# Performance work log

Hardware: AMD Instinct MI355X
Metric: run time of the kernel (lower is better)

Reference implementation:

```python
import jax, jax.numpy as jnp
import numpy as np

B, T, F, H, S = 4096, 200, 76, 128, 17


def setup_inputs() -> dict:
    key = jax.random.key(0)
    ks = jax.random.split(key, 10)
    kf = 1.0 / np.sqrt(H)
    return {
        "x": jax.random.normal(ks[0], (B, T, F), dtype=jnp.float32),
        "static": jax.random.normal(ks[1], (B, S), dtype=jnp.float32),
        "h0": jax.random.normal(ks[2], (B, H), dtype=jnp.float32),
        "c0": jax.random.normal(ks[3], (B, H), dtype=jnp.float32),
        "W_ih": jax.random.uniform(ks[4], (4 * H, F), jnp.float32, -kf, kf),
        "W_hh": jax.random.uniform(ks[5], (4 * H, H), jnp.float32, -kf, kf),
        "b_ih": jax.random.uniform(ks[6], (4 * H,), jnp.float32, -kf, kf),
        "b_hh": jax.random.uniform(ks[7], (4 * H,), jnp.float32, -kf, kf),
        "W_lin": jax.random.uniform(ks[8], (1, H + S), jnp.float32, -kf, kf),
        "b_lin": jax.random.uniform(ks[9], (1,), jnp.float32, -kf, kf),
    }


def reference(x, static, h0, c0, W_ih, W_hh, b_ih, b_hh, W_lin, b_lin):
    # Precompute input projections for all timesteps in one big GEMM: [B,T,4H]
    x_proj = jnp.einsum("btf,gf->btg", x, W_ih) + b_ih
    xs = jnp.swapaxes(x_proj, 0, 1)  # time-major [T, B, 4H]

    def step(carry, xp):
        h, c = carry
        gates = xp + h @ W_hh.T + b_hh  # [B, 4H]
        i, f, g, o = jnp.split(gates, 4, axis=-1)
        i, f, o = jax.nn.sigmoid(i), jax.nn.sigmoid(f), jax.nn.sigmoid(o)
        c = f * c + i * jnp.tanh(g)
        h = o * jnp.tanh(c)
        return (h, c), None

    (h, c), _ = jax.lax.scan(step, (h0, c0), xs)
    full = jnp.concatenate([h, static], axis=1)  # [B, H+S]
    predictions = full @ W_lin.T + b_lin  # [B, 1]
    return predictions
```

## Files before the change

kernel.cpp:

```cpp
#include <hip/hip_runtime.h>
#include <hip/hip_bf16.h>

#define B_TOT   4096
#define T_LEN   200
#define F_IN    76
#define H_DIM   128
#define S_DIM   17
#define BLK_B   16
#define NTHREADS 512
#define NT_CHUNK 8
#define NCHUNK  (T_LEN / NT_CHUNK)
#define XPITCH  96
#define HPITCH  136
#define ROW_F4  ((NT_CHUNK * F_IN) / 4)
#define PF_N    5

static_assert(NCHUNK * NT_CHUNK == T_LEN, "chunking must cover T exactly");

using f32x4 = __attribute__((ext_vector_type(4))) float;
using s16x8 = __attribute__((ext_vector_type(8))) short;

#if __has_builtin(__builtin_amdgcn_exp2f)
#define EXP2(v) __builtin_amdgcn_exp2f(v)
#else
#define EXP2(v) exp2f(v)
#endif
#if __has_builtin(__builtin_amdgcn_rcpf)
#define RCP(v) __builtin_amdgcn_rcpf(v)
#else
#define RCP(v) (1.0f / (v))
#endif

__device__ __forceinline__ short f2bf(float f) {
    union { float f; unsigned u; } v; v.f = f;
    unsigned r = v.u + 0x7FFFu + ((v.u >> 16) & 1u);
    return (short)(r >> 16);
}
__device__ __forceinline__ float bf2f(short s) {
    union { unsigned u; float f; } v;
    v.u = ((unsigned)(unsigned short)s) << 16;
    return v.f;
}
__device__ __forceinline__ unsigned cvt_pk_bf16(float lo, float hi) {
    unsigned r;
    asm("v_cvt_pk_bf16_f32 %0, %1, %2" : "=v"(r) : "v"(lo), "v"(hi));
    return r;
}

__global__ __launch_bounds__(NTHREADS, 2) void lstm_fused(
    const float* __restrict__ x,    const float* __restrict__ stat,
    const float* __restrict__ h0,   const float* __restrict__ c0,
    const float* __restrict__ W_ih, const float* __restrict__ W_hh,
    const float* __restrict__ b_ih, const float* __restrict__ b_hh,
    const float* __restrict__ W_lin, const float* __restrict__ b_lin,
    float* __restrict__ out)
{
    __shared__ __align__(16) short xbuf[2][NT_CHUNK][BLK_B][XPITCH];
    __shared__ __align__(16) short hbuf[2][BLK_B][HPITCH];

    const int tid  = threadIdx.x;
    const int lane = tid & 63;
    const int wave = tid >> 6;
    const int lrow = lane & 15;
    const int lk8  = (lane >> 4) << 3;
    const int r0   = (lane >> 4) << 2;
    const int b0   = blockIdx.x * BLK_B;
    const int hb   = wave << 4;

    const float C1 = 1.44269504088896f;
    const float gs[4] = { -C1, -C1, -2.0f * C1, -C1 };

    s16x8 wih[4][3], whh[4][4];
    float bias[4];
#pragma unroll
    for (int nt = 0; nt < 4; ++nt) {
        const int col = nt * H_DIM + hb + lrow;
        const float s = gs[nt];
#pragma unroll
        for (int kt = 0; kt < 3; ++kt) {
            s16x8 f;
#pragma unroll
            for (int j = 0; j < 8; ++j) {
                int k = kt * 32 + lk8 + j;
                float v = (k < F_IN) ? W_ih[col * F_IN + k] * s : 0.0f;
                f[j] = f2bf(v);
            }
            wih[nt][kt] = f;
        }
#pragma unroll
        for (int kt = 0; kt < 4; ++kt) {
            s16x8 f;
#pragma unroll
            for (int j = 0; j < 8; ++j) {
                int k = kt * 32 + lk8 + j;
                f[j] = f2bf(W_hh[col * H_DIM + k] * s);
            }
            whh[nt][kt] = f;
        }
        bias[nt] = (b_ih[col] + b_hh[col]) * s;
    }

    float c[4];
#pragma unroll
    for (int r = 0; r < 4; ++r)
        c[r] = c0[(b0 + r0 + r) * H_DIM + hb + lrow];

    for (int i = tid; i < BLK_B * H_DIM; i += NTHREADS) {
        int row = i >> 7, cc = i & 127;
        hbuf[0][row][cc] = f2bf(h0[(b0 + row) * H_DIM + cc]);
    }
    for (int i = tid; i < 2 * NT_CHUNK * BLK_B * (XPITCH - F_IN); i += NTHREADS) {
        int rem = i;
        int f   = rem % (XPITCH - F_IN); rem /= (XPITCH - F_IN);
        int row = rem % BLK_B;           rem /= BLK_B;
        int tt  = rem % NT_CHUNK;        rem /= NT_CHUNK;
        xbuf[rem][tt][row][F_IN + f] = 0;
    }

    const int prow = tid >> 5;
    const int pidx = tid & 31;
    const float* psrc = x + (size_t)(b0 + prow) * (T_LEN * F_IN) + pidx * 4;
    int ldsoff[PF_N];
#pragma unroll
    for (int i = 0; i < PF_N; ++i) {
        int s4 = pidx + 32 * i;
        int q  = 4 * s4;
        int tp = (q * 863) >> 16;
        int f0 = q - 76 * tp;
        ldsoff[i] = (tp * BLK_B + prow) * XPITCH + f0;
    }

    f32x4 pf[PF_N];
    auto issue = [&](int ch) {
        const float* p = psrc + (size_t)ch * (NT_CHUNK * F_IN);
#pragma unroll
        for (int i = 0; i < PF_N; ++i)
            if (i < PF_N - 1 || pidx < ROW_F4 - 4 * 32)
                pf[i] = *(const f32x4*)(p + i * 128);
    };
    auto commit = [&](int buf) {
        short* xb0 = &xbuf[buf][0][0][0];
#pragma unroll
        for (int i = 0; i < PF_N; ++i)
            if (i < PF_N - 1 || pidx < ROW_F4 - 4 * 32) {
                unsigned lo = cvt_pk_bf16(pf[i].x, pf[i].y);
                unsigned hi = cvt_pk_bf16(pf[i].z, pf[i].w);
                unsigned long long v = ((unsigned long long)hi << 32) | lo;
                *(unsigned long long*)(xb0 + ldsoff[i]) = v;
            }
    };

    issue(0);
    commit(0);
    __syncthreads();

    s16x8 axr[3];
    f32x4 xa[4];
    auto load_ax = [&](int buf, int tt) {
#pragma unroll
        for (int kt = 0; kt < 3; ++kt)
            axr[kt] = *(const s16x8*)&xbuf[buf][tt][lrow][kt * 32 + lk8];
    };
    auto calc_xa = [&]() {
#pragma unroll
        for (int nt = 0; nt < 4; ++nt) {
            f32x4 t = (f32x4){ bias[nt], bias[nt], bias[nt], bias[nt] };
#pragma unroll
            for (int kt = 0; kt < 3; ++kt)
                t = __builtin_amdgcn_mfma_f32_16x16x32_bf16(axr[kt], wih[nt][kt], t, 0, 0, 0);
            xa[nt] = t;
        }
    };

    load_ax(0, 0);
    calc_xa();

#define STEP(CUR, TT)                                                          \
    {                                                                          \
        s16x8 ah[4];                                                           \
        _Pragma("unroll")                                                      \
        for (int kt = 0; kt < 4; ++kt)                                         \
            ah[kt] = *(const s16x8*)&hbuf[CUR][lrow][kt * 32 + lk8];           \
        f32x4 acc[4];                                                          \
        _Pragma("unroll")                                                      \
        for (int nt = 0; nt < 4; ++nt) {                                       \
            f32x4 t = xa[nt];                                                  \
            _Pragma("unroll")                                                  \
            for (int kt = 0; kt < 4; ++kt)                                     \
                t = __builtin_amdgcn_mfma_f32_16x16x32_bf16(ah[kt], whh[nt][kt], t, 0, 0, 0); \
            acc[nt] = t;                                                       \
        }                                                                      \
        if ((TT) < NT_CHUNK - 1) { load_ax(xc, (TT) + 1); calc_xa(); }         \
        float hv[4];                                                           \
        _Pragma("unroll")                                                      \
        for (int r = 0; r < 4; ++r) {                                          \
            float A  = EXP2(acc[0][r]);                                        \
            float Bv = EXP2(acc[1][r]);                                        \
            float E  = EXP2(acc[2][r]);                                        \
            float Dv = EXP2(acc[3][r]);                                        \
            float sE = 1.f - E, p3 = 1.f + E;                                  \
            float p1 = 1.f + A, p2 = 1.f + Bv;                                 \
            float q13 = p1 * p3;                                               \
            float num = fmaf(c[r], q13, sE * p2);                              \
            float cn  = num * RCP(q13 * p2);                                   \
            c[r] = cn;                                                         \
            float ea = fminf(cn * (-2.f * C1), 80.f);                          \
            float Ec = EXP2(ea);                                               \
            float sEc = 1.f - Ec, uEc = 1.f + Ec;                              \
            hv[r] = sEc * RCP((1.f + Dv) * uEc);                               \
        }                                                                      \
        if ((TT) == 0 && ch + 1 < NCHUNK) issue(ch + 1);                       \
        if ((TT) == NT_CHUNK - 1 && ch + 1 < NCHUNK) commit(xc ^ 1);           \
        unsigned q01 = cvt_pk_bf16(hv[0], hv[1]);                              \
        unsigned q23 = cvt_pk_bf16(hv[2], hv[3]);                              \
        unsigned short* hp = (unsigned short*)&hbuf[(CUR) ^ 1][r0][hb + lrow]; \
        hp[0 * HPITCH] = (unsigned short)q01;                                  \
        hp[1 * HPITCH] = (unsigned short)(q01 >> 16);                          \
        hp[2 * HPITCH] = (unsigned short)q23;                                  \
        hp[3 * HPITCH] = (unsigned short)(q23 >> 16);                          \
        __syncthreads();                                                       \
        if ((TT) == NT_CHUNK - 1 && ch + 1 < NCHUNK) {                         \
            load_ax(xc ^ 1, 0); calc_xa();                                     \
        }                                                                      \
    }

    for (int ch = 0; ch < NCHUNK; ++ch) {
        const int xc = ch & 1;
        for (int tt = 0; tt < NT_CHUNK; tt += 2) {
            STEP(0, tt)
            STEP(1, tt + 1)
        }
    }
#undef STEP

    if (tid < BLK_B) {
        const int row = tid;
        float a = b_lin[0];
        for (int k = 0; k < H_DIM; ++k)
            a += bf2f(hbuf[0][row][k]) * W_lin[k];
        for (int s = 0; s < S_DIM; ++s)
            a += stat[(b0 + row) * S_DIM + s] * W_lin[H_DIM + s];
        out[b0 + row] = a;
    }
}

extern "C" void kernel_launch(void* const* d_in, const int* in_sizes, int n_in,
                              void* d_out, int out_size, void* d_ws, size_t ws_size,
                              hipStream_t stream) {
    const float* xx   = (const float*)d_in[0];
    const float* st   = (const float*)d_in[1];
    const float* h0   = (const float*)d_in[2];
    const float* c0   = (const float*)d_in[3];
    const float* Wih  = (const float*)d_in[4];
    const float* Whh  = (const float*)d_in[5];
    const float* bih  = (const float*)d_in[6];
    const float* bhh  = (const float*)d_in[7];
    const float* Wlin = (const float*)d_in[8];
    const float* blin = (const float*)d_in[9];
    float* o = (float*)d_out;

    lstm_fused<<<B_TOT / BLK_B, NTHREADS, 0, stream>>>(
        xx, st, h0, c0, Wih, Whh, bih, bhh, Wlin, blin, o);
}
```

Measured before the change: 207.9 us.

## Interleave input-projection MFMAs with gate nonlinearities and use raw LDS barrier

Splits the next-step input projection (REBUILD) per gate tile and interleaves it with the per-row nonlinearity computations. The aim is to overlap MFMA latency with transcendental VALU work. The x-tile LDS load is issued earlier, before the recurrent MFMAs, and the h stores are split so half can be written early. The time loop over each chunk is fully unrolled, and __syncthreads is replaced by a raw s_waitcnt lgkmcnt(0) + s_barrier, which risks missing waits on global memory operations.

```diff
diff --git a/kernel.cpp b/kernel.cpp
--- a/kernel.cpp
+++ b/kernel.cpp
@@ -47,6 +47,8 @@
     return r;
 }
 
+#define LDS_BARRIER() asm volatile("s_waitcnt lgkmcnt(0)\n\ts_barrier" ::: "memory")
+
 __global__ __launch_bounds__(NTHREADS, 2) void lstm_fused(
     const float* __restrict__ x,    const float* __restrict__ stat,
     const float* __restrict__ h0,   const float* __restrict__ c0,
@@ -71,7 +73,7 @@
     const float gs[4] = { -C1, -C1, -2.0f * C1, -C1 };
 
     s16x8 wih[4][3], whh[4][4];
-    float bias[4];
+    f32x4 biasf[4];
 #pragma unroll
     for (int nt = 0; nt < 4; ++nt) {
         const int col = nt * H_DIM + hb + lrow;
@@ -97,7 +99,8 @@
             }
             whh[nt][kt] = f;
         }
-        bias[nt] = (b_ih[col] + b_hh[col]) * s;
+        float bv = (b_ih[col] + b_hh[col]) * s;
+        biasf[nt] = (f32x4){ bv, bv, bv, bv };
     }
 
     float c[4];
@@ -161,77 +164,85 @@
         for (int kt = 0; kt < 3; ++kt)
             axr[kt] = *(const s16x8*)&xbuf[buf][tt][lrow][kt * 32 + lk8];
     };
-    auto calc_xa = [&]() {
-#pragma unroll
-        for (int nt = 0; nt < 4; ++nt) {
-            f32x4 t = (f32x4){ bias[nt], bias[nt], bias[nt], bias[nt] };
-#pragma unroll
-            for (int kt = 0; kt < 3; ++kt)
-                t = __builtin_amdgcn_mfma_f32_16x16x32_bf16(axr[kt], wih[nt][kt], t, 0, 0, 0);
-            xa[nt] = t;
-        }
-    };
+
+#define REBUILD(NT)                                                              \
+    xa[NT] = __builtin_amdgcn_mfma_f32_16x16x32_bf16(axr[2], wih[NT][2],         \
+             __builtin_amdgcn_mfma_f32_16x16x32_bf16(axr[1], wih[NT][1],         \
+             __builtin_amdgcn_mfma_f32_16x16x32_bf16(axr[0], wih[NT][0],         \
+             biasf[NT], 0, 0, 0), 0, 0, 0), 0, 0, 0)
+
+#define NONLIN(R)                                                                \
+    {   float A  = EXP2(acc[0][R]);                                              \
+        float Bv = EXP2(acc[1][R]);                                              \
+        float E  = EXP2(acc[2][R]);                                              \
+        float Dv = EXP2(acc[3][R]);                                              \
+        float p1 = 1.f + A, p2 = 1.f + Bv, p3 = 1.f + E;                         \
+        float q13 = p1 * p3;                                                     \
+        float num = fmaf(c[R], q13, (1.f - E) * p2);                             \
+        float cn  = num * RCP(q13 * p2);                                         \
+        c[R] = cn;                                                               \
+        float Ec  = EXP2(fminf(cn * (-2.f * C1), 80.f));                         \
+        hv[R] = (1.f - Ec) * RCP((1.f + Dv) * (1.f + Ec)); }
 
     load_ax(0, 0);
-    calc_xa();
-
-#define STEP(CUR, TT)                                                          \
-    {                                                                          \
-        s16x8 ah[4];                                                           \
-        _Pragma("unroll")                                                      \
-        for (int kt = 0; kt < 4; ++kt)                                         \
-            ah[kt] = *(const s16x8*)&hbuf[CUR][lrow][kt * 32 + lk8];           \
-        f32x4 acc[4];                                                          \
-        _Pragma("unroll")                                                      \
-        for (int nt = 0; nt < 4; ++nt) {                                       \
-            f32x4 t = xa[nt];                                                  \
-            _Pragma("unroll")                                                  \
-            for (int kt = 0; kt < 4; ++kt)                                     \
-                t = __builtin_amdgcn_mfma_f32_16x16x32_bf16(ah[kt], whh[nt][kt], t, 0, 0, 0); \
-            acc[nt] = t;                                                       \
-        }                                                                      \
-        if ((TT) < NT_CHUNK - 1) { load_ax(xc, (TT) + 1); calc_xa(); }         \
-        float hv[4];                                                           \
-        _Pragma("unroll")                                                      \
-        for (int r = 0; r < 4; ++r) {                                          \
-            float A  = EXP2(acc[0][r]);                                        \
-            float Bv = EXP2(acc[1][r]);                                        \
-            float E  = EXP2(acc[2][r]);                                        \
-            float Dv = EXP2(acc[3][r]);                                        \
-            float sE = 1.f - E, p3 = 1.f + E;                                  \
-            float p1 = 1.f + A, p2 = 1.f + Bv;                                 \
-            float q13 = p1 * p3;                                               \
-            float num = fmaf(c[r], q13, sE * p2);                              \
-            float cn  = num * RCP(q13 * p2);                                   \
-            c[r] = cn;                                                         \
-            float ea = fminf(cn * (-2.f * C1), 80.f);                          \
-            float Ec = EXP2(ea);                                               \
-            float sEc = 1.f - Ec, uEc = 1.f + Ec;                              \
-            hv[r] = sEc * RCP((1.f + Dv) * uEc);                               \
-        }                                                                      \
-        if ((TT) == 0 && ch + 1 < NCHUNK) issue(ch + 1);                       \
-        if ((TT) == NT_CHUNK - 1 && ch + 1 < NCHUNK) commit(xc ^ 1);           \
-        unsigned q01 = cvt_pk_bf16(hv[0], hv[1]);                              \
-        unsigned q23 = cvt_pk_bf16(hv[2], hv[3]);                              \
-        unsigned short* hp = (unsigned short*)&hbuf[(CUR) ^ 1][r0][hb + lrow]; \
-        hp[0 * HPITCH] = (unsigned short)q01;                                  \
-        hp[1 * HPITCH] = (unsigned short)(q01 >> 16);                          \
-        hp[2 * HPITCH] = (unsigned short)q23;                                  \
-        hp[3 * HPITCH] = (unsigned short)(q23 >> 16);                          \
-        __syncthreads();                                                       \
-        if ((TT) == NT_CHUNK - 1 && ch + 1 < NCHUNK) {                         \
-            load_ax(xc ^ 1, 0); calc_xa();                                     \
-        }                                                                      \
-    }
-
+    REBUILD(0); REBUILD(1); REBUILD(2); REBUILD(3);
+
+#define STEP(CUR, TT)                                                            \
+    {                                                                            \
+        s16x8 ah[4];                                                             \
+        _Pragma("unroll")                                                        \
+        for (int kt = 0; kt < 4; ++kt)                                           \
+            ah[kt] = *(const s16x8*)&hbuf[CUR][lrow][kt * 32 + lk8];             \
+        if ((TT) < NT_CHUNK - 1) load_ax(xc, (TT) + 1);                          \
+        f32x4 acc[4];                                                            \
+        _Pragma("unroll")                                                        \
+        for (int nt = 0; nt < 4; ++nt) {                                         \
+            f32x4 t = __builtin_amdgcn_mfma_f32_16x16x32_bf16(ah[0], whh[nt][0], xa[nt], 0, 0, 0); \
+            t = __builtin_amdgcn_mfma_f32_16x16x32_bf16(ah[1], whh[nt][1], t, 0, 0, 0); \
+            t = __builtin_amdgcn_mfma_f32_16x16x32_bf16(ah[2], whh[nt][2], t, 0, 0, 0); \
+            t = __builtin_amdgcn_mfma_f32_16x16x32_bf16(ah[3], whh[nt][3], t, 0, 0, 0); \
+            acc[nt] = t;                                                         \
+        }                                                                        \
+        if ((TT) == 0 && ch + 1 < NCHUNK) issue(ch + 1);                         \
+        float hv[4];                                                             \
+        unsigned short* hp = (unsigned short*)&hbuf[(CUR) ^ 1][r0][hb + lrow];   \
+        NONLIN(0);                                                               \
+        if ((TT) < NT_CHUNK - 1) { REBUILD(0); }                                 \
+        NONLIN(1);                                                               \
+        {   unsigned q01 = cvt_pk_bf16(hv[0], hv[1]);                            \
+            hp[0 * HPITCH] = (unsigned short)q01;                                \
+            hp[1 * HPITCH] = (unsigned short)(q01 >> 16); }                      \
+        if ((TT) < NT_CHUNK - 1) { REBUILD(1); }                                 \
+        NONLIN(2);                                                               \
+        if ((TT) < NT_CHUNK - 1) { REBUILD(2); }                                 \
+        NONLIN(3);                                                               \
+        {   unsigned q23 = cvt_pk_bf16(hv[2], hv[3]);                            \
+            hp[2 * HPITCH] = (unsigned short)q23;                                \
+            hp[3 * HPITCH] = (unsigned short)(q23 >> 16); }                      \
+        if ((TT) < NT_CHUNK - 1) { REBUILD(3); }                                 \
+        if ((TT) == NT_CHUNK - 1 && ch + 1 < NCHUNK) commit(xc ^ 1);             \
+        LDS_BARRIER();                                                           \
+    }
+
+#pragma unroll 1
     for (int ch = 0; ch < NCHUNK; ++ch) {
         const int xc = ch & 1;
-        for (int tt = 0; tt < NT_CHUNK; tt += 2) {
-            STEP(0, tt)
-            STEP(1, tt + 1)
+        STEP(0, 0)
+        STEP(1, 1)
+        STEP(0, 2)
+        STEP(1, 3)
+        STEP(0, 4)
+        STEP(1, 5)
+        STEP(0, 6)
+        STEP(1, 7)
+        if (ch + 1 < NCHUNK) {
+            load_ax(xc ^ 1, 0);
+            REBUILD(0); REBUILD(1); REBUILD(2); REBUILD(3);
         }
     }
 #undef STEP
+#undef NONLIN
+#undef REBUILD
 
     if (tid < BLK_B) {
         const int row = tid;
```

Result: no change. 205.6 us (-1.1%).
